# Performance work log

Measured on AMD Instinct MI355X. Metric: run time of the kernel, lower is better.

## Reference

```python
import jax, jax.numpy as jnp
import numpy as np
from jax import lax

DIM, HEADS, DIM_HEAD = 768, 12, 64
INNER = HEADS * DIM_HEAD
DIM_ROT = 32
FH = FW = 32
N = 1 + FH * FW
B = 8


def setup_inputs() -> dict:
    key = jax.random.key(0)
    ks = jax.random.split(key, 8)
    s = 0.02
    return {
        "x": jax.random.normal(ks[0], (B, N, DIM), jnp.float32),
        "sin": jax.random.normal(ks[1], (N - 1, DIM_ROT), jnp.float32),
        "cos": jax.random.normal(ks[2], (N - 1, DIM_ROT), jnp.float32),
        "ln_g": jnp.ones((DIM,), jnp.float32),
        "ln_b": jnp.zeros((DIM,), jnp.float32),
        "dw_w": jax.random.normal(ks[3], (DIM, 1, 5, 5), jnp.float32) * s,
        "pw_w": jax.random.normal(ks[4], (INNER, DIM, 1, 1), jnp.float32) * s,
        "kv_w": jax.random.normal(ks[5], (DIM, 2 * INNER), jnp.float32) * s,
        "out_w": jax.random.normal(ks[6], (INNER, DIM), jnp.float32) * s,
        "out_b": jnp.zeros((DIM,), jnp.float32),
        "fmap_h": FH,
        "fmap_w": FW,
    }


def _rotate_every_two(t):
    # (..., d) with pairs (x1, x2) -> (-x2, x1)
    shp = t.shape
    t = t.reshape(*shp[:-1], -1, 2)
    x1, x2 = t[..., 0], t[..., 1]
    return jnp.stack((-x2, x1), axis=-1).reshape(shp)


def _layernorm(x, g, b, eps=1e-5):
    mu = jnp.mean(x, -1, keepdims=True)
    var = jnp.var(x, -1, keepdims=True)
    return (x - mu) * lax.rsqrt(var + eps) * g + b


def reference(x, sin, cos, ln_g, ln_b, dw_w, pw_w, kv_w, out_w, out_b, fmap_h, fmap_w):
    b, n, _ = x.shape
    scale = DIM_HEAD ** -0.5
    xn = _layernorm(x, ln_g, ln_b)

    # --- query path: SpatialConv (depthwise 5x5 + 1x1), cls via Identity ---
    cls_tok, spatial = xn[:, :1], xn[:, 1:]
    fmap = spatial.reshape(b, fmap_h, fmap_w, DIM).transpose(0, 3, 1, 2)  # NCHW
    fmap = lax.conv_general_dilated(
        fmap, dw_w, window_strides=(1, 1), padding=[(2, 2), (2, 2)],
        dimension_numbers=("NCHW", "OIHW", "NCHW"), feature_group_count=DIM)
    fmap = lax.conv_general_dilated(
        fmap, pw_w, window_strides=(1, 1), padding="VALID",
        dimension_numbers=("NCHW", "OIHW", "NCHW"))
    q = fmap.transpose(0, 2, 3, 1).reshape(b, fmap_h * fmap_w, INNER)
    q = jnp.concatenate((cls_tok, q), axis=1)  # cls_proj is Identity (dim==inner)

    # --- kv projection ---
    kv = xn @ kv_w
    k, v = kv[..., :INNER], kv[..., INNER:]

    def to_heads(t):  # b n (h d) -> (b h) n d
        return t.reshape(b, n, HEADS, DIM_HEAD).transpose(0, 2, 1, 3).reshape(b * HEADS, n, DIM_HEAD)

    q, k, v = map(to_heads, (q, k, v))

    # --- partial rotary, skipping cls token ---
    def apply_rot(t):
        t_cls, t_sp = t[:, :1], t[:, 1:]
        t_rot, t_pass = t_sp[..., :DIM_ROT], t_sp[..., DIM_ROT:]
        t_rot = t_rot * cos + _rotate_every_two(t_rot) * sin
        return jnp.concatenate((t_cls, jnp.concatenate((t_rot, t_pass), -1)), axis=1)

    q, k = apply_rot(q), apply_rot(k)

    dots = jnp.einsum("bid,bjd->bij", q, k) * scale
    attn = jax.nn.softmax(dots, axis=-1)
    out = jnp.einsum("bij,bjd->bid", attn, v)
    out = out.reshape(b, HEADS, n, DIM_HEAD).transpose(0, 2, 1, 3).reshape(b, n, INNER)
    return out @ out_w + out_b
```

## Files before the change

kernel.cpp:

```cpp
#include <hip/hip_runtime.h>
#include <cstddef>

#define NSEQ   1025
#define NBATCH 8
#define NTOK   8200
#define DIMX   768
#define NHEADS 12
#define DHEAD  64
#define VTP3   8320
#define LDP    72
#define CP     136

typedef short bf16x8 __attribute__((ext_vector_type(8)));
typedef float f32x4  __attribute__((ext_vector_type(4)));
typedef unsigned short u16;

__device__ __forceinline__ float bf2f(u16 u) {
    unsigned v = (unsigned)u << 16; float f; __builtin_memcpy(&f, &v, 4); return f;
}
__device__ __forceinline__ u16 f2bf(float f) {
    unsigned u; __builtin_memcpy(&u, &f, 4);
    return (u16)((u + 0x7FFFu + ((u >> 16) & 1u)) >> 16);
}

__device__ __forceinline__ void gl2lds16(const u16* g, u16* l) {
    __builtin_amdgcn_global_load_lds((__attribute__((address_space(1))) void*)g,
                                     (__attribute__((address_space(3))) void*)l, 16, 0, 0);
}

__launch_bounds__(256)
__global__ void ln_pre_kernel(const float* __restrict__ x, const float* __restrict__ g,
                              const float* __restrict__ bb, u16* __restrict__ xn,
                              u16* __restrict__ qout,
                              const float* __restrict__ dw_w, const float* __restrict__ pw_w,
                              const float* __restrict__ kv_w, const float* __restrict__ out_w,
                              float* __restrict__ dwT, u16* __restrict__ pw_bf,
                              u16* __restrict__ kv_wT, u16* __restrict__ out_wT)
{
    __shared__ float red[8];
    __shared__ float stats[2];
    __shared__ float tile[32][33];
    int tid = threadIdx.x;
    if (blockIdx.x < NTOK) {
        int t = blockIdx.x;
        const float* xp = x + (size_t)t * DIMX;
        float v0 = xp[tid], v1 = xp[tid + 256], v2 = xp[tid + 512];
        float s  = v0 + v1 + v2;
        float ss = v0*v0 + v1*v1 + v2*v2;
        for (int off = 32; off > 0; off >>= 1) {
            s  += __shfl_down(s,  off, 64);
            ss += __shfl_down(ss, off, 64);
        }
        int w = tid >> 6, lane = tid & 63;
        if (lane == 0) { red[w] = s; red[4 + w] = ss; }
        __syncthreads();
        if (tid == 0) {
            float S  = red[0] + red[1] + red[2] + red[3];
            float SS = red[4] + red[5] + red[6] + red[7];
            float mu  = S * (1.0f / DIMX);
            float var = SS * (1.0f / DIMX) - mu * mu;
            stats[0] = mu; stats[1] = rsqrtf(var + 1e-5f);
        }
        __syncthreads();
        float mu = stats[0], rs = stats[1];
        float y0 = (v0 - mu) * rs * g[tid]       + bb[tid];
        float y1 = (v1 - mu) * rs * g[tid + 256] + bb[tid + 256];
        float y2 = (v2 - mu) * rs * g[tid + 512] + bb[tid + 512];
        u16* op = xn + (size_t)t * DIMX;
        op[tid] = f2bf(y0); op[tid + 256] = f2bf(y1); op[tid + 512] = f2bf(y2);
        int bq = t / NSEQ;
        if (t == bq * NSEQ) {
            int c0 = tid, c1 = tid + 256, c2 = tid + 512;
            qout[((size_t)(bq * NHEADS + (c0 >> 6)) * NSEQ) * DHEAD + (c0 & 63)] = f2bf(y0 * 0.125f);
            qout[((size_t)(bq * NHEADS + (c1 >> 6)) * NSEQ) * DHEAD + (c1 & 63)] = f2bf(y1 * 0.125f);
            qout[((size_t)(bq * NHEADS + (c2 >> 6)) * NSEQ) * DHEAD + (c2 & 63)] = f2bf(y2 * 0.125f);
        }
        return;
    }
    int blk = blockIdx.x - NTOK;
    if (blk < 75) {
        int idx = blk * 256 + tid;
        if (idx < 768 * 25) {
            int c = idx / 25, wi = idx % 25;
            dwT[wi * 768 + c] = dw_w[idx];
        }
        return;
    }
    if (blk < 2379) {
        int i = (blk - 75) * 256 + tid;
        pw_bf[i] = f2bf(pw_w[i]);
        return;
    }
    const float* in; u16* out; int R, C, bx, by;
    if (blk < 3531) {
        int t2 = blk - 2379; bx = t2 % 48; by = t2 / 48;
        in = kv_w; out = kv_wT; R = 768; C = 1536;
    } else {
        int t2 = blk - 3531; bx = t2 % 24; by = t2 / 24;
        in = out_w; out = out_wT; R = 768; C = 768;
    }
    int tx = tid & 31, ty = tid >> 5;
    int xg = bx * 32 + tx, y0 = by * 32;
    for (int i = ty; i < 32; i += 8)
        tile[i][tx] = in[(size_t)(y0 + i) * C + xg];
    __syncthreads();
    int xo = by * 32 + tx, yo0 = bx * 32;
    for (int i = ty; i < 32; i += 8)
        out[(size_t)(yo0 + i) * R + xo] = f2bf(tile[tx][i]);
}

__launch_bounds__(256)
__global__ void dw_kernel(const u16* __restrict__ xn, const float* __restrict__ wt,
                          u16* __restrict__ out)
{
    int gid = blockIdx.x * 256 + threadIdx.x;
    int pix = gid / 96, cg = gid - pix * 96;
    int c = cg * 8;
    int b = pix >> 10, p = pix & 1023, y = p >> 5, x0 = p & 31;
    float acc[8] = {};
    for (int dy = 0; dy < 5; dy++) {
        int yy = y + dy - 2;
        if ((unsigned)yy >= 32u) continue;
        for (int dx = 0; dx < 5; dx++) {
            int xx = x0 + dx - 2;
            if ((unsigned)xx >= 32u) continue;
            const u16* ip = xn + ((size_t)(b * NSEQ) + 1 + yy * 32 + xx) * DIMX + c;
            uint4 iv = *(const uint4*)ip;
            const float* wp = wt + (dy * 5 + dx) * DIMX + c;
            float4 w0 = *(const float4*)wp;
            float4 w1 = *(const float4*)(wp + 4);
            acc[0] += bf2f((u16)(iv.x & 0xFFFFu)) * w0.x;
            acc[1] += bf2f((u16)(iv.x >> 16))     * w0.y;
            acc[2] += bf2f((u16)(iv.y & 0xFFFFu)) * w0.z;
            acc[3] += bf2f((u16)(iv.y >> 16))     * w0.w;
            acc[4] += bf2f((u16)(iv.z & 0xFFFFu)) * w1.x;
            acc[5] += bf2f((u16)(iv.z >> 16))     * w1.y;
            acc[6] += bf2f((u16)(iv.w & 0xFFFFu)) * w1.z;
            acc[7] += bf2f((u16)(iv.w >> 16))     * w1.w;
        }
    }
    uint4 ov;
    ov.x = (unsigned)f2bf(acc[0]) | ((unsigned)f2bf(acc[1]) << 16);
    ov.y = (unsigned)f2bf(acc[2]) | ((unsigned)f2bf(acc[3]) << 16);
    ov.z = (unsigned)f2bf(acc[4]) | ((unsigned)f2bf(acc[5]) << 16);
    ov.w = (unsigned)f2bf(acc[6]) | ((unsigned)f2bf(acc[7]) << 16);
    *(uint4*)(out + (size_t)pix * DIMX + c) = ov;
}

__launch_bounds__(256)
__global__ void gemm_proj(const u16* __restrict__ xn, const u16* __restrict__ dwout,
                          const u16* __restrict__ kvT, const u16* __restrict__ pwB,
                          u16* __restrict__ kOut, u16* __restrict__ VtOut,
                          u16* __restrict__ qOut,
                          const float* __restrict__ sinb, const float* __restrict__ cosb)
{
    __shared__ u16 smem[128 * CP];
    u16* As = smem;
    u16* Bs = smem + 8192;
    const int tid  = threadIdx.x;
    const int wave = tid >> 6, lane = tid & 63;
    const int q8 = lane >> 4, cc = lane & 15;
    const int wr = wave >> 1, wc = wave & 1;

    int bid = blockIdx.x;
    int mode, c0;
    long r0;
    const u16 *A, *Bn;
    if (bid < 390)      { mode = 0; c0 = (bid % 6) * 128;  r0 = (long)(bid / 6) * 128;  A = xn;              Bn = kvT; }
    else if (bid < 780) { int t2 = bid - 390;
                          mode = 2; c0 = (t2 % 65) * 128;  r0 = (long)(t2 / 65) * 128; A = kvT + 768 * 768; Bn = xn; }
    else                { int t2 = bid - 780;
                          mode = 1; c0 = (t2 % 6) * 128;   r0 = (long)(t2 / 6) * 128;  A = dwout;           Bn = pwB; }

    f32x4 acc[4][4] = {};

    for (int k0 = 0; k0 < 768; k0 += 64) {
        __syncthreads();
        #pragma unroll
        for (int p = 0; p < 4; p++) {
            int chunk = wave * 256 + p * 64 + lane;
            int row = chunk >> 3, cs = chunk & 7;
            int src = cs ^ (row & 7);
            long brow;
            if (mode == 2) {
                int s = c0 + row;
                int bb2 = s / 1032;
                brow = (long)bb2 * NSEQ + (s - bb2 * 1032);
            } else brow = c0 + row;
            const u16* ga = A  + (size_t)(r0 + row) * 768 + k0 + src * 8;
            const u16* gb = Bn + (size_t)brow * 768 + k0 + src * 8;
            u16* la = As + (size_t)(wave * 256 + p * 64) * 8;
            u16* lb = Bs + (size_t)(wave * 256 + p * 64) * 8;
            gl2lds16(ga, la);
            gl2lds16(gb, lb);
        }
        __syncthreads();
        #pragma unroll
        for (int ks = 0; ks < 2; ks++) {
            const int chsw = (((ks * 4 + q8) ^ (cc & 7)) * 8);
            bf16x8 af[4], bfr[4];
            #pragma unroll
            for (int mi = 0; mi < 4; mi++)
                af[mi] = *(const bf16x8*)(As + (wr * 64 + mi * 16 + cc) * 64 + chsw);
            #pragma unroll
            for (int ni = 0; ni < 4; ni++)
                bfr[ni] = *(const bf16x8*)(Bs + (wc * 64 + ni * 16 + cc) * 64 + chsw);
            #pragma unroll
            for (int mi = 0; mi < 4; mi++)
                #pragma unroll
                for (int ni = 0; ni < 4; ni++)
                    acc[mi][ni] = __builtin_amdgcn_mfma_f32_16x16x32_bf16(af[mi], bfr[ni], acc[mi][ni], 0, 0, 0);
        }
    }

    __syncthreads();
    #pragma unroll
    for (int mi = 0; mi < 4; mi++)
        #pragma unroll
        for (int r = 0; r < 4; r++) {
            int lr = wr * 64 + mi * 16 + q8 * 4 + r;
            #pragma unroll
            for (int ni = 0; ni < 4; ni++)
                smem[lr * CP + wc * 64 + ni * 16 + cc] = f2bf(acc[mi][ni][r]);
        }
    __syncthreads();

    if (mode == 2) {
        #pragma unroll
        for (int p = 0; p < 8; p++) {
            int id = p * 256 + tid;
            int row = id >> 4, c8 = (id & 15) * 8;
            uint4 val = *(const uint4*)(smem + row * CP + c8);
            *(uint4*)(VtOut + (size_t)(r0 + row) * VTP3 + c0 + c8) = val;
        }
        return;
    }

    #pragma unroll
    for (int p = 0; p < 8; p++) {
        int id = p * 256 + tid;
        int row = id >> 4, c8 = (id & 15) * 8;
        long grow = r0 + row;
        if (grow >= ((mode == 1) ? 8192 : NTOK)) continue;
        uint4 val = *(const uint4*)(smem + row * CP + c8);
        int b, n;
        if (mode == 1) { b = (int)(grow >> 10); n = (int)(grow & 1023) + 1; }
        else           { b = (int)(grow / NSEQ); n = (int)(grow % NSEQ); }
        int c2 = c0 + c8;
        u16* dst = (mode == 1) ? qOut : kOut;
        int d0 = c2 & 63;
        {
            u16 e[8];
            unsigned wv[4] = {val.x, val.y, val.z, val.w};
            #pragma unroll
            for (int j = 0; j < 4; j++) { e[2*j] = (u16)(wv[j] & 0xFFFFu); e[2*j+1] = (u16)(wv[j] >> 16); }
            bool doro = (d0 < 32) && (n >= 1);
            if (mode == 1 || doro) {
                float f[8];
                #pragma unroll
                for (int j = 0; j < 8; j++) f[j] = bf2f(e[j]);
                if (mode == 1) {
                    #pragma unroll
                    for (int j = 0; j < 8; j++) f[j] *= 0.125f;
                }
                if (doro) {
                    int pos = n - 1;
                    const float* cp = cosb + pos * 32 + d0;
                    const float* sp = sinb + pos * 32 + d0;
                    float4 cv0 = *(const float4*)cp, cv1 = *(const float4*)(cp + 4);
                    float4 sv0 = *(const float4*)sp, sv1 = *(const float4*)(sp + 4);
                    float ca[8] = {cv0.x, cv0.y, cv0.z, cv0.w, cv1.x, cv1.y, cv1.z, cv1.w};
                    float sa[8] = {sv0.x, sv0.y, sv0.z, sv0.w, sv1.x, sv1.y, sv1.z, sv1.w};
                    #pragma unroll
                    for (int pr = 0; pr < 4; pr++) {
                        float a = f[2*pr], bb2 = f[2*pr+1];
                        f[2*pr]   = a   * ca[2*pr]   - bb2 * sa[2*pr];
                        f[2*pr+1] = bb2 * ca[2*pr+1] + a   * sa[2*pr+1];
                    }
                }
                #pragma unroll
                for (int j = 0; j < 8; j++) e[j] = f2bf(f[j]);
            }
            #pragma unroll
            for (int j = 0; j < 4; j++) wv[j] = (unsigned)e[2*j] | ((unsigned)e[2*j+1] << 16);
            val = make_uint4(wv[0], wv[1], wv[2], wv[3]);
        }
        *(uint4*)(dst + ((size_t)(b * NHEADS + (c2 >> 6)) * NSEQ + n) * DHEAD + (c2 & 63)) = val;
    }
}

__launch_bounds__(256)
__global__ void gemm_out(const u16* __restrict__ A, const u16* __restrict__ Bn,
                         const float* __restrict__ bias, float* __restrict__ Of, int M)
{
    __shared__ u16 smem[16384];
    u16* As = smem;
    u16* Bs = smem + 8192;
    const int tid  = threadIdx.x;
    const int wave = tid >> 6, lane = tid & 63;
    const int q8 = lane >> 4, cc = lane & 15;
    const int wr = wave >> 1, wc = wave & 1;
    const long r0 = (long)blockIdx.y * 128;
    const int  c0 = blockIdx.x * 128;

    f32x4 acc[4][4] = {};

    for (int k0 = 0; k0 < 768; k0 += 64) {
        __syncthreads();
        #pragma unroll
        for (int p = 0; p < 4; p++) {
            int chunk = wave * 256 + p * 64 + lane;
            int row = chunk >> 3, cs = chunk & 7;
            int src = cs ^ (row & 7);
            const u16* ga = A  + (size_t)(r0 + row) * 768 + k0 + src * 8;
            const u16* gb = Bn + (size_t)(c0 + row) * 768 + k0 + src * 8;
            u16* la = As + (size_t)(wave * 256 + p * 64) * 8;
            u16* lb = Bs + (size_t)(wave * 256 + p * 64) * 8;
            gl2lds16(ga, la);
            gl2lds16(gb, lb);
        }
        __syncthreads();
        #pragma unroll
        for (int ks = 0; ks < 2; ks++) {
            const int chsw = (((ks * 4 + q8) ^ (cc & 7)) * 8);
            bf16x8 af[4], bfr[4];
            #pragma unroll
            for (int mi = 0; mi < 4; mi++)
                af[mi] = *(const bf16x8*)(As + (wr * 64 + mi * 16 + cc) * 64 + chsw);
            #pragma unroll
            for (int ni = 0; ni < 4; ni++)
                bfr[ni] = *(const bf16x8*)(Bs + (wc * 64 + ni * 16 + cc) * 64 + chsw);
            #pragma unroll
            for (int mi = 0; mi < 4; mi++)
                #pragma unroll
                for (int ni = 0; ni < 4; ni++)
                    acc[mi][ni] = __builtin_amdgcn_mfma_f32_16x16x32_bf16(af[mi], bfr[ni], acc[mi][ni], 0, 0, 0);
        }
    }
    #pragma unroll
    for (int mi = 0; mi < 4; mi++) {
        #pragma unroll
        for (int r = 0; r < 4; r++) {
            long row = r0 + wr * 64 + mi * 16 + q8 * 4 + r;
            if (row >= M) continue;
            #pragma unroll
            for (int ni = 0; ni < 4; ni++) {
                int col = c0 + wc * 64 + ni * 16 + cc;
                Of[(size_t)row * 768 + col] = acc[mi][ni][r] + bias[col];
            }
        }
    }
}

__launch_bounds__(512)
__global__ void attn_kernel(const u16* __restrict__ q, const u16* __restrict__ k,
                            const u16* __restrict__ Vt, u16* __restrict__ o)
{
    __shared__ u16 Kb[2][4096];
    __shared__ u16 Vb[2][4096];
    __shared__ u16 Ps[8 * 16 * LDP];
    const int tid  = threadIdx.x;
    const int wave = tid >> 6, lane = tid & 63;
    const int q8 = lane >> 4, cc = lane & 15;
    const int bh = blockIdx.x;
    const int i0 = blockIdx.y * 128;
    const int b = bh / NHEADS, h = bh % NHEADS;
    const size_t kbase = (size_t)bh * NSEQ * 64;
    const size_t vbase = (size_t)(h * 64) * VTP3 + (size_t)b * 1032;

    bf16x8 aq[2];
    {
        const u16* qp = q + kbase + (size_t)(i0 + wave * 16 + cc) * 64;
        aq[0] = *(const bf16x8*)(qp + q8 * 8);
        aq[1] = *(const bf16x8*)(qp + 32 + q8 * 8);
    }

    auto stage = [&](int jt, int buf) {
        int j0 = jt * 64;
        int chunk = wave * 64 + lane;
        int row = chunk >> 3, cs = chunk & 7;
        int src = cs ^ (row & 7);
        gl2lds16(k  + kbase + (size_t)(j0 + row) * 64 + src * 8, Kb[buf] + wave * 512);
        gl2lds16(Vt + vbase + (size_t)row * VTP3 + j0 + src * 8,  Vb[buf] + wave * 512);
    };

    stage(0, 0);
    f32x4 O[4] = {};
    float lsum[4] = {0.f, 0.f, 0.f, 0.f};
    u16* Psw = Ps + wave * 16 * LDP;

    for (int jt = 0; jt < 17; jt++) {
        __syncthreads();
        const u16* Kc = Kb[jt & 1];
        const u16* Vc = Vb[jt & 1];
        if (jt < 16) stage(jt + 1, (jt + 1) & 1);

        f32x4 sf[4] = {};
        #pragma unroll
        for (int ks = 0; ks < 2; ks++) {
            #pragma unroll
            for (int ni = 0; ni < 4; ni++) {
                bf16x8 bk = *(const bf16x8*)(Kc + (ni * 16 + cc) * 64 + (((ks * 4 + q8) ^ (cc & 7)) * 8));
                sf[ni] = __builtin_amdgcn_mfma_f32_16x16x32_bf16(aq[ks], bk, sf[ni], 0, 0, 0);
            }
        }

        bool mask = (jt == 16);
        #pragma unroll
        for (int ni = 0; ni < 4; ni++)
            #pragma unroll
            for (int r = 0; r < 4; r++) {
                float p = __expf(sf[ni][r]);
                if (mask && (ni * 16 + cc != 0)) p = 0.f;
                lsum[r] += p;
                unsigned u; __builtin_memcpy(&u, &p, 4);
                Psw[(q8 * 4 + r) * LDP + ni * 16 + cc] = (u16)((u + 0x8000u) >> 16);
            }

        #pragma unroll
        for (int ks = 0; ks < 2; ks++) {
            bf16x8 pa = *(const bf16x8*)(Psw + cc * LDP + ks * 32 + q8 * 8);
            #pragma unroll
            for (int ni = 0; ni < 4; ni++) {
                bf16x8 vb = *(const bf16x8*)(Vc + (ni * 16 + cc) * 64 + (((ks * 4 + q8) ^ (cc & 7)) * 8));
                O[ni] = __builtin_amdgcn_mfma_f32_16x16x32_bf16(pa, vb, O[ni], 0, 0, 0);
            }
        }
    }

    #pragma unroll
    for (int r = 0; r < 4; r++) {
        lsum[r] += __shfl_xor(lsum[r], 1, 64);
        lsum[r] += __shfl_xor(lsum[r], 2, 64);
        lsum[r] += __shfl_xor(lsum[r], 4, 64);
        lsum[r] += __shfl_xor(lsum[r], 8, 64);
    }
    #pragma unroll
    for (int r = 0; r < 4; r++) {
        int i = i0 + wave * 16 + q8 * 4 + r;
        if (i >= NSEQ) continue;
        float inv = 1.0f / lsum[r];
        #pragma unroll
        for (int ni = 0; ni < 4; ni++)
            o[((size_t)(b * NSEQ + i)) * 768 + h * 64 + ni * 16 + cc] = f2bf(O[ni][r] * inv);
    }
}

extern "C" void kernel_launch(void* const* d_in, const int* in_sizes, int n_in,
                              void* d_out, int out_size, void* d_ws, size_t ws_size,
                              hipStream_t stream)
{
    const float* x     = (const float*)d_in[0];
    const float* sinb  = (const float*)d_in[1];
    const float* cosb  = (const float*)d_in[2];
    const float* ln_g  = (const float*)d_in[3];
    const float* ln_b  = (const float*)d_in[4];
    const float* dw_w  = (const float*)d_in[5];
    const float* pw_w  = (const float*)d_in[6];
    const float* kv_w  = (const float*)d_in[7];
    const float* out_w = (const float*)d_in[8];
    const float* out_b = (const float*)d_in[9];
    (void)in_sizes; (void)n_in; (void)out_size; (void)ws_size;

    u16* ws = (u16*)d_ws;
    u16* xn_bf    = ws;
    u16* dwout_bf = ws + 6297600;
    u16* q_bf     = ws + 12589056;
    u16* k_bf     = ws + 18886656;
    u16* Vt       = ws + 25184256;
    u16* pw_bf    = ws + 31574016;
    u16* kv_wT    = ws + 32163840;
    u16* out_wT   = ws + 33343488;
    float* dwT    = (float*)(ws + 33933312);
    u16* attn_bf  = xn_bf;

    ln_pre_kernel <<<NTOK + 4107, 256, 0, stream>>>(x, ln_g, ln_b, xn_bf, q_bf,
                                                    dw_w, pw_w, kv_w, out_w,
                                                    dwT, pw_bf, kv_wT, out_wT);
    dw_kernel     <<<3072, 256, 0, stream>>>(xn_bf, dwT, dwout_bf);
    gemm_proj     <<<1164, 256, 0, stream>>>(xn_bf, dwout_bf, kv_wT, pw_bf,
                                             k_bf, Vt, q_bf, sinb, cosb);
    attn_kernel   <<<dim3(96, 9), 512, 0, stream>>>(q_bf, k_bf, Vt, attn_bf);
    gemm_out      <<<dim3(6, 65), 256, 0, stream>>>(attn_bf, out_wT, out_b, (float*)d_out, NTOK);
}
```

Before: 274.3 us.

## Double attention query rows per wave and handle tail row in dedicated block

Each wave now processes 32 query rows (two 16-row MFMA tiles), so a block covers 256 queries and each staged K/V tile serves twice as many rows. The lone 1025th query row moves to a separate scalar block (blockIdx.y==4) that computes its dot products, softmax sum and PV product with plain FP32 loops. The grid shrinks from 9 to 5 row-blocks per head, which cuts redundant K/V loads from global memory. In exchange each thread holds more registers and there are fewer blocks in flight, and the tail block's scalar path may become a straggler.

```diff
diff --git a/kernel.cpp b/kernel.cpp
--- a/kernel.cpp
+++ b/kernel.cpp
@@ -358,21 +358,77 @@
 {
     __shared__ u16 Kb[2][4096];
     __shared__ u16 Vb[2][4096];
-    __shared__ u16 Ps[8 * 16 * LDP];
+    __shared__ u16 Ps[8 * 32 * LDP];
     const int tid  = threadIdx.x;
     const int wave = tid >> 6, lane = tid & 63;
     const int q8 = lane >> 4, cc = lane & 15;
     const int bh = blockIdx.x;
-    const int i0 = blockIdx.y * 128;
     const int b = bh / NHEADS, h = bh % NHEADS;
     const size_t kbase = (size_t)bh * NSEQ * 64;
     const size_t vbase = (size_t)(h * 64) * VTP3 + (size_t)b * 1032;
 
-    bf16x8 aq[2];
-    {
-        const u16* qp = q + kbase + (size_t)(i0 + wave * 16 + cc) * 64;
-        aq[0] = *(const bf16x8*)(qp + q8 * 8);
-        aq[1] = *(const bf16x8*)(qp + 32 + q8 * 8);
+    if (blockIdx.y == 4) {
+        float* qs  = (float*)Ps;
+        float* Pj  = qs + 64;
+        float* Op  = Pj + 1032;
+        float* red = Op + 512;
+        if (tid < 64) qs[tid] = bf2f(q[kbase + (size_t)1024 * 64 + tid]);
+        __syncthreads();
+        float lp = 0.f;
+        #pragma unroll
+        for (int jj = 0; jj < 2; jj++) {
+            int j = tid + jj * 512;
+            const u16* kr = k + kbase + (size_t)j * 64;
+            float dot = 0.f;
+            #pragma unroll
+            for (int d8 = 0; d8 < 8; d8++) {
+                uint4 kv = *(const uint4*)(kr + d8 * 8);
+                unsigned wv[4] = {kv.x, kv.y, kv.z, kv.w};
+                #pragma unroll
+                for (int e = 0; e < 4; e++) {
+                    dot += bf2f((u16)(wv[e] & 0xFFFFu)) * qs[d8 * 8 + e * 2];
+                    dot += bf2f((u16)(wv[e] >> 16))     * qs[d8 * 8 + e * 2 + 1];
+                }
+            }
+            float p = __expf(dot);
+            Pj[j] = p; lp += p;
+        }
+        if (tid == 0) {
+            const u16* kr = k + kbase + (size_t)1024 * 64;
+            float dot = 0.f;
+            for (int d = 0; d < 64; d++) dot += bf2f(kr[d]) * qs[d];
+            float p = __expf(dot);
+            Pj[1024] = p; lp += p;
+        }
+        for (int off = 32; off > 0; off >>= 1) lp += __shfl_down(lp, off, 64);
+        if (lane == 0) red[wave] = lp;
+        __syncthreads();
+        {
+            int d = tid & 63, w = tid >> 6;
+            int jbeg = w * 128, jend = (w == 7) ? 1025 : jbeg + 128;
+            const u16* vr = Vt + (size_t)(h * 64 + d) * VTP3 + (size_t)b * 1032;
+            float acc = 0.f;
+            for (int j = jbeg; j < jend; j++) acc += Pj[j] * bf2f(vr[j]);
+            Op[w * 64 + d] = acc;
+        }
+        __syncthreads();
+        if (tid < 64) {
+            float s = 0.f, lsum = 0.f;
+            #pragma unroll
+            for (int w = 0; w < 8; w++) { s += Op[w * 64 + tid]; lsum += red[w]; }
+            o[((size_t)(b * NSEQ + 1024)) * 768 + h * 64 + tid] = f2bf(s / lsum);
+        }
+        return;
+    }
+
+    const int i0 = blockIdx.y * 256;
+
+    bf16x8 aq[2][2];
+    #pragma unroll
+    for (int mi = 0; mi < 2; mi++) {
+        const u16* qp = q + kbase + (size_t)(i0 + wave * 32 + mi * 16 + cc) * 64;
+        aq[mi][0] = *(const bf16x8*)(qp + q8 * 8);
+        aq[mi][1] = *(const bf16x8*)(qp + 32 + q8 * 8);
     }
 
     auto stage = [&](int jt, int buf) {
@@ -385,9 +441,9 @@
     };
 
     stage(0, 0);
-    f32x4 O[4] = {};
-    float lsum[4] = {0.f, 0.f, 0.f, 0.f};
-    u16* Psw = Ps + wave * 16 * LDP;
+    f32x4 O[2][4] = {};
+    float lsum[2][4] = {};
+    u16* Psw = Ps + wave * 32 * LDP;
 
     for (int jt = 0; jt < 17; jt++) {
         __syncthreads();
@@ -395,55 +451,67 @@
         const u16* Vc = Vb[jt & 1];
         if (jt < 16) stage(jt + 1, (jt + 1) & 1);
 
-        f32x4 sf[4] = {};
+        f32x4 sf[2][4] = {};
         #pragma unroll
         for (int ks = 0; ks < 2; ks++) {
             #pragma unroll
             for (int ni = 0; ni < 4; ni++) {
                 bf16x8 bk = *(const bf16x8*)(Kc + (ni * 16 + cc) * 64 + (((ks * 4 + q8) ^ (cc & 7)) * 8));
-                sf[ni] = __builtin_amdgcn_mfma_f32_16x16x32_bf16(aq[ks], bk, sf[ni], 0, 0, 0);
+                #pragma unroll
+                for (int mi = 0; mi < 2; mi++)
+                    sf[mi][ni] = __builtin_amdgcn_mfma_f32_16x16x32_bf16(aq[mi][ks], bk, sf[mi][ni], 0, 0, 0);
             }
         }
 
         bool mask = (jt == 16);
         #pragma unroll
-        for (int ni = 0; ni < 4; ni++)
-            #pragma unroll
-            for (int r = 0; r < 4; r++) {
-                float p = __expf(sf[ni][r]);
-                if (mask && (ni * 16 + cc != 0)) p = 0.f;
-                lsum[r] += p;
-                unsigned u; __builtin_memcpy(&u, &p, 4);
-                Psw[(q8 * 4 + r) * LDP + ni * 16 + cc] = (u16)((u + 0x8000u) >> 16);
-            }
+        for (int mi = 0; mi < 2; mi++)
+            #pragma unroll
+            for (int ni = 0; ni < 4; ni++)
+                #pragma unroll
+                for (int r = 0; r < 4; r++) {
+                    float p = __expf(sf[mi][ni][r]);
+                    if (mask && (ni * 16 + cc != 0)) p = 0.f;
+                    lsum[mi][r] += p;
+                    unsigned u; __builtin_memcpy(&u, &p, 4);
+                    Psw[(mi * 16 + q8 * 4 + r) * LDP + ni * 16 + cc] = (u16)((u + 0x8000u) >> 16);
+                }
 
         #pragma unroll
         for (int ks = 0; ks < 2; ks++) {
-            bf16x8 pa = *(const bf16x8*)(Psw + cc * LDP + ks * 32 + q8 * 8);
+            bf16x8 pa[2];
+            #pragma unroll
+            for (int mi = 0; mi < 2; mi++)
+                pa[mi] = *(const bf16x8*)(Psw + (mi * 16 + cc) * LDP + ks * 32 + q8 * 8);
             #pragma unroll
             for (int ni = 0; ni < 4; ni++) {
                 bf16x8 vb = *(const bf16x8*)(Vc + (ni * 16 + cc) * 64 + (((ks * 4 + q8) ^ (cc & 7)) * 8));
-                O[ni] = __builtin_amdgcn_mfma_f32_16x16x32_bf16(pa, vb, O[ni], 0, 0, 0);
+                #pragma unroll
+                for (int mi = 0; mi < 2; mi++)
+                    O[mi][ni] = __builtin_amdgcn_mfma_f32_16x16x32_bf16(pa[mi], vb, O[mi][ni], 0, 0, 0);
             }
         }
     }
 
     #pragma unroll
-    for (int r = 0; r < 4; r++) {
-        lsum[r] += __shfl_xor(lsum[r], 1, 64);
-        lsum[r] += __shfl_xor(lsum[r], 2, 64);
-        lsum[r] += __shfl_xor(lsum[r], 4, 64);
-        lsum[r] += __shfl_xor(lsum[r], 8, 64);
-    }
+    for (int mi = 0; mi < 2; mi++)
+        #pragma unroll
+        for (int r = 0; r < 4; r++) {
+            lsum[mi][r] += __shfl_xor(lsum[mi][r], 1, 64);
+            lsum[mi][r] += __shfl_xor(lsum[mi][r], 2, 64);
+            lsum[mi][r] += __shfl_xor(lsum[mi][r], 4, 64);
+            lsum[mi][r] += __shfl_xor(lsum[mi][r], 8, 64);
+        }
     #pragma unroll
-    for (int r = 0; r < 4; r++) {
-        int i = i0 + wave * 16 + q8 * 4 + r;
-        if (i >= NSEQ) continue;
-        float inv = 1.0f / lsum[r];
-        #pragma unroll
-        for (int ni = 0; ni < 4; ni++)
-            o[((size_t)(b * NSEQ + i)) * 768 + h * 64 + ni * 16 + cc] = f2bf(O[ni][r] * inv);
-    }
+    for (int mi = 0; mi < 2; mi++)
+        #pragma unroll
+        for (int r = 0; r < 4; r++) {
+            int i = i0 + wave * 32 + mi * 16 + q8 * 4 + r;
+            float inv = 1.0f / lsum[mi][r];
+            #pragma unroll
+            for (int ni = 0; ni < 4; ni++)
+                o[((size_t)(b * NSEQ + i)) * 768 + h * 64 + ni * 16 + cc] = f2bf(O[mi][ni][r] * inv);
+        }
 }
 
 extern "C" void kernel_launch(void* const* d_in, const int* in_sizes, int n_in,
@@ -480,6 +548,6 @@
     dw_kernel     <<<3072, 256, 0, stream>>>(xn_bf, dwT, dwout_bf);
     gemm_proj     <<<1164, 256, 0, stream>>>(xn_bf, dwout_bf, kv_wT, pw_bf,
                                              k_bf, Vt, q_bf, sinb, cosb);
-    attn_kernel   <<<dim3(96, 9), 512, 0, stream>>>(q_bf, k_bf, Vt, attn_bf);
+    attn_kernel   <<<dim3(96, 5), 512, 0, stream>>>(q_bf, k_bf, Vt, attn_bf);
     gemm_out      <<<dim3(6, 65), 256, 0, stream>>>(attn_bf, out_wT, out_b, (float*)d_out, NTOK);
 }
```

Result: slower. 288.5 us (+5.2%).
